# Kernel optimization log

Hardware: AMD Instinct MI355X
Metric: run time of the kernel (lower is better)

The kernel has to match this reference:

```python
import jax, jax.numpy as jnp
import numpy as np

TOP_K = 32
TEMPERATURE = 1.0
PARAM_SCALE = 0.02


def setup_inputs() -> dict:
    key = jax.random.key(0)
    ks = jax.random.split(key, 7)
    B, S, D, F, P, R = 2, 1024, 1024, 4096, 256, 64
    x = jax.random.normal(ks[0], (B, S, D), dtype=jnp.float32)
    fc1_A = jax.random.normal(ks[1], (P, D, R), dtype=jnp.float32) * PARAM_SCALE
    fc1_B = jax.random.normal(ks[2], (P, R, F), dtype=jnp.float32) * PARAM_SCALE
    fc2_A = jax.random.normal(ks[3], (P, F, R), dtype=jnp.float32) * PARAM_SCALE
    fc2_B = jax.random.normal(ks[4], (P, R, D), dtype=jnp.float32) * PARAM_SCALE
    fc1_logits = jax.random.normal(ks[5], (P,), dtype=jnp.float32)
    fc2_logits = jax.random.normal(ks[6], (P,), dtype=jnp.float32)
    return {"x": x, "fc1_A": fc1_A, "fc1_B": fc1_B, "fc2_A": fc2_A,
            "fc2_B": fc2_B, "fc1_logits": fc1_logits, "fc2_logits": fc2_logits}


def _compose_weight(logits, A, B):
    """Top-k select primitives, softmax composition weights, weighted low-rank sum.

    A: (P, d_in, r), B: (P, r, d_out) -> W: (d_in, d_out)
    """
    vals, idx = jax.lax.top_k(logits, TOP_K)          # (K,), (K,)
    w = jax.nn.softmax(vals / TEMPERATURE)            # composition weights over selected
    A_sel = A[idx]                                    # (K, d_in, r) gather
    B_sel = B[idx]                                    # (K, r, d_out) gather
    return jnp.einsum('k,kir,kro->io', w, A_sel, B_sel)


def reference(x, fc1_A, fc1_B, fc2_A, fc2_B, fc1_logits, fc2_logits):
    W1 = _compose_weight(fc1_logits, fc1_A, fc1_B)    # (D, F)
    W2 = _compose_weight(fc2_logits, fc2_A, fc2_B)    # (F, D)
    h = jax.nn.gelu(jnp.einsum('bsd,df->bsf', x, W1))
    return jnp.einsum('bsf,fd->bsd', h, W2)
```

## Files before the change

kernel.cpp:

```cpp
#include <hip/hip_runtime.h>
#include <cstdint>
#include <cstddef>

typedef __attribute__((ext_vector_type(8))) short bhalf8;
typedef __attribute__((ext_vector_type(4))) float f32x4;

__device__ __forceinline__ unsigned short f2bf(float f){
    unsigned int u = __float_as_uint(f);
    u += 0x7fffu + ((u >> 16) & 1u);
    return (unsigned short)(u >> 16);
}

__device__ __forceinline__ float gelu_tanh(float x){
    const float c1 = 2.302584f;
    float y  = x + 0.044715f * x * x * x;
    float e  = __builtin_amdgcn_exp2f(c1 * y);
    float r  = __builtin_amdgcn_rcpf(e + 1.0f);
    return x - x * r;
}

__device__ __forceinline__ void async_lds16(const unsigned short* g, unsigned short* l){
    __builtin_amdgcn_global_load_lds(
        (const __attribute__((address_space(1))) void*)g,
        (__attribute__((address_space(3))) void*)l, 16, 0, 0);
}

__global__ void topk_softmax_kernel(const float* __restrict__ lg1,
                                    const float* __restrict__ lg2,
                                    int* __restrict__ idx_out,
                                    float* __restrict__ w_out)
{
    const float* lg = (blockIdx.x == 0) ? lg1 : lg2;
    int*   idxo = idx_out + blockIdx.x * 32;
    float* wo   = w_out   + blockIdx.x * 32;
    const int lane = threadIdx.x;
    float v[4];
    #pragma unroll
    for (int j = 0; j < 4; ++j) v[j] = lg[lane * 4 + j];
    __shared__ float svals[32];
    for (int k = 0; k < 32; ++k){
        float bv = -1e30f; int bi = 0;
        #pragma unroll
        for (int j = 0; j < 4; ++j){
            if (v[j] > bv){ bv = v[j]; bi = lane * 4 + j; }
        }
        for (int off = 32; off > 0; off >>= 1){
            float ov = __shfl_down(bv, off);
            int   oi = __shfl_down(bi, off);
            if (ov > bv){ bv = ov; bi = oi; }
        }
        bi = __shfl(bi, 0);
        if (lane == 0){ svals[k] = bv; idxo[k] = bi; }
        if ((bi >> 2) == lane) v[bi & 3] = -1e30f;
    }
    float sv = svals[lane & 31];
    float e  = expf(sv - svals[0]);
    float s  = e;
    #pragma unroll
    for (int off = 16; off > 0; off >>= 1) s += __shfl_xor(s, off);
    if (lane < 32) wo[lane] = e / s;
}

__global__ void prep_gather_kernel(const float* __restrict__ x,  unsigned short* __restrict__ x16,
                                   const float* __restrict__ fc1A, unsigned short* __restrict__ Ag1,
                                   const float* __restrict__ fc1B, unsigned short* __restrict__ Bt1,
                                   const float* __restrict__ fc2A, unsigned short* __restrict__ Ag2,
                                   const float* __restrict__ fc2B, unsigned short* __restrict__ Bg2t,
                                   const int* __restrict__ idxb, const float* __restrict__ wb)
{
    __shared__ float tile[64][65];
    const int t = threadIdx.x;
    int b = blockIdx.x;

    if (b < 2048){
        int v = b * 256 + t;
        float4 xx = ((const float4*)x)[v];
        ushort4 o; o.x=f2bf(xx.x); o.y=f2bf(xx.y); o.z=f2bf(xx.z); o.w=f2bf(xx.w);
        ((ushort4*)x16)[v] = o;
        return;
    }
    b -= 2048;
    if (b < 10240){
        const float* src; unsigned short* dst; const int* idx; const float* w;
        int Drows, use_scale, v;
        if (b < 2048){ src=fc1A; dst=Ag1; idx=idxb;    w=wb;    Drows=1024; use_scale=1; v=b*256+t; }
        else         { src=fc2A; dst=Ag2; idx=idxb+32; w=wb+32; Drows=4096; use_scale=0; v=(b-2048)*256+t; }
        int c4 = v & 511;
        int d  = v >> 9;
        int k  = c4 >> 4;
        int r4 = c4 & 15;
        int p  = idx[k];
        float sc = use_scale ? w[k] : 1.0f;
        float4 xx = *((const float4*)(src + ((size_t)p * Drows + d) * 64) + r4);
        ushort4 o;
        o.x = f2bf(sc * xx.x); o.y = f2bf(sc * xx.y);
        o.z = f2bf(sc * xx.z); o.w = f2bf(sc * xx.w);
        *(ushort4*)(dst + (size_t)d * 2048 + k * 64 + r4 * 4) = o;
        return;
    }
    b -= 10240;
    const float* src; unsigned short* dst; const int* idx; const float* w;
    int Fcols, use_scale;
    if (b < 2048){ src=fc1B; dst=Bt1;  idx=idxb;    w=wb;    Fcols=4096; use_scale=0; }
    else         { src=fc2B; dst=Bg2t; idx=idxb+32; w=wb+32; Fcols=1024; use_scale=1; b -= 2048; }
    const int k  = b & 31;
    const int f0 = (b >> 5) * 64;
    const int p  = idx[k];
    const float sc = use_scale ? w[k] : 1.0f;
    const int cf = t & 15;
    const int r0 = t >> 4;
    #pragma unroll
    for (int pass = 0; pass < 4; ++pass){
        int r = r0 + pass * 16;
        float4 xx = *((const float4*)(src + ((size_t)p * 64 + r) * Fcols + f0) + cf);
        tile[r][cf * 4 + 0] = xx.x; tile[r][cf * 4 + 1] = xx.y;
        tile[r][cf * 4 + 2] = xx.z; tile[r][cf * 4 + 3] = xx.w;
    }
    __syncthreads();
    const int r4  = t & 15;
    const int fl0 = t >> 4;
    #pragma unroll
    for (int pass = 0; pass < 4; ++pass){
        int fl = fl0 + pass * 16;
        ushort4 o;
        o.x = f2bf(sc * tile[r4 * 4 + 0][fl]);
        o.y = f2bf(sc * tile[r4 * 4 + 1][fl]);
        o.z = f2bf(sc * tile[r4 * 4 + 2][fl]);
        o.w = f2bf(sc * tile[r4 * 4 + 3][fl]);
        *(ushort4*)(dst + (size_t)(f0 + fl) * 2048 + k * 64 + r4 * 4) = o;
    }
}

template<int EPI>
__device__ __forceinline__ void gemm_body(unsigned short* smem,
                                          const unsigned short* __restrict__ A,
                                          const unsigned short* __restrict__ Bt,
                                          void* __restrict__ Cout,
                                          int N, int K, int Kslice, int kbeg,
                                          int bm, int bn)
{
    const int t    = threadIdx.x;
    const int wave = t >> 6;
    const int lane = t & 63;
    const int wr   = (wave >> 1) * 64;
    const int wc   = (wave & 1) * 64;
    const int m16  = lane & 15;
    const int quad = lane >> 4;
    const int srow = t >> 2;
    const int scol = t & 3;

    f32x4 acc[4][4];
    const f32x4 z = {0.f, 0.f, 0.f, 0.f};
    #pragma unroll
    for (int i = 0; i < 4; ++i)
        #pragma unroll
        for (int j = 0; j < 4; ++j) acc[i][j] = z;

    const unsigned short* Arow = A  + (size_t)(bm + srow) * K + scol * 8 + kbeg;
    const unsigned short* Brow = Bt + (size_t)(bn + srow) * K + scol * 8 + kbeg;
    const size_t rstep = (size_t)64 * K;

    auto stage = [&](int slot, int k0){
        unsigned short* s = smem + slot * 16384 + t * 8;
        async_lds16(Arow + k0,              s);
        async_lds16(Arow + rstep + k0,      s + 2048);
        async_lds16(Arow + k0 + 32,         s + 4096);
        async_lds16(Arow + rstep + k0 + 32, s + 6144);
        async_lds16(Brow + k0,              s + 8192);
        async_lds16(Brow + rstep + k0,      s + 10240);
        async_lds16(Brow + k0 + 32,         s + 12288);
        async_lds16(Brow + rstep + k0 + 32, s + 14336);
    };

    const int nIter = Kslice >> 6;

    stage(0, 0);
    asm volatile("s_waitcnt vmcnt(0)" ::: "memory");
    __builtin_amdgcn_s_barrier();

    for (int it = 0; it < nIter; ++it){
        unsigned short* sb = smem + (it & 1) * 16384;
        if (it + 1 < nIter) stage((it + 1) & 1, (it + 1) * 64);

        bhalf8 af0[4], bf0[4], af1[4], bf1[4];
        #pragma unroll
        for (int i = 0; i < 4; ++i){
            af0[i] = *(const bhalf8*)(sb +         (wr + i * 16 + m16) * 32 + quad * 8);
            af1[i] = *(const bhalf8*)(sb + 4096  + (wr + i * 16 + m16) * 32 + quad * 8);
        }
        #pragma unroll
        for (int j = 0; j < 4; ++j){
            bf0[j] = *(const bhalf8*)(sb + 8192  + (wc + j * 16 + m16) * 32 + quad * 8);
            bf1[j] = *(const bhalf8*)(sb + 12288 + (wc + j * 16 + m16) * 32 + quad * 8);
        }

        #pragma unroll
        for (int i = 0; i < 4; ++i)
            #pragma unroll
            for (int j = 0; j < 4; ++j)
                acc[i][j] = __builtin_amdgcn_mfma_f32_16x16x32_bf16(af0[i], bf0[j], acc[i][j], 0, 0, 0);
        #pragma unroll
        for (int i = 0; i < 4; ++i)
            #pragma unroll
            for (int j = 0; j < 4; ++j)
                acc[i][j] = __builtin_amdgcn_mfma_f32_16x16x32_bf16(af1[i], bf1[j], acc[i][j], 0, 0, 0);

        if (it + 1 < nIter){
            asm volatile("s_waitcnt vmcnt(0) lgkmcnt(0)" ::: "memory");
            __builtin_amdgcn_s_barrier();
        }
    }

    #pragma unroll
    for (int i = 0; i < 4; ++i){
        #pragma unroll
        for (int j = 0; j < 4; ++j){
            #pragma unroll
            for (int r = 0; r < 4; ++r){
                int row = bm + wr + i * 16 + quad * 4 + r;
                int col = bn + wc + j * 16 + m16;
                float vv = acc[i][j][r];
                if (EPI == 1) vv = gelu_tanh(vv);
                if (EPI == 2) ((float*)Cout)[(size_t)row * N + col] = vv;
                else ((unsigned short*)Cout)[(size_t)row * N + col] = f2bf(vv);
            }
        }
    }
}

__device__ __forceinline__ int xcd_swz512(int id){ return (id & 7) * 64 + (id >> 3); }

__launch_bounds__(256, 2)
__global__ void gemm13_kernel(const unsigned short* __restrict__ A1,
                              const unsigned short* __restrict__ B1,
                              unsigned short* __restrict__ C1,
                              const unsigned short* __restrict__ A2,
                              const unsigned short* __restrict__ B2,
                              unsigned short* __restrict__ C2)
{
    __shared__ unsigned short smem[2 * 16384];
    int id = xcd_swz512(blockIdx.x);
    if (id < 256){
        gemm_body<0>(smem, A1, B1, C1, 1024, 2048, 2048, 0,
                     (id >> 3) * 128, (id & 7) * 128);
    } else {
        id -= 256;
        gemm_body<0>(smem, A2, B2, C2, 4096, 2048, 2048, 0,
                     (id >> 5) * 128, (id & 31) * 128);
    }
}

__launch_bounds__(256, 2)
__global__ void gemm2_kernel(const unsigned short* __restrict__ A,
                             const unsigned short* __restrict__ Bt,
                             unsigned short* __restrict__ C)
{
    __shared__ unsigned short smem[2 * 16384];
    int id = xcd_swz512(blockIdx.x);
    gemm_body<1>(smem, A, Bt, C, 4096, 1024, 1024, 0,
                 (id >> 5) * 128, (id & 31) * 128);
}

__launch_bounds__(256, 2)
__global__ void gemm4_kernel(const unsigned short* __restrict__ A,
                             const unsigned short* __restrict__ Bt,
                             float* __restrict__ part)
{
    __shared__ unsigned short smem[2 * 16384];
    int id = xcd_swz512(blockIdx.x);
    int bz = id >> 7;
    int r  = id & 127;
    float* Cs = part + (size_t)bz * (2048 * 1024);
    gemm_body<2>(smem, A, Bt, Cs, 1024, 4096, 1024, bz * 1024,
                 (r >> 3) * 128, (r & 7) * 128);
}

__global__ void reduce4_kernel(const float4* __restrict__ p, float4* __restrict__ out)
{
    const int S = 524288;
    int v = blockIdx.x * 256 + threadIdx.x;
    float4 a = p[v], b = p[v + S], c = p[v + 2 * S], d = p[v + 3 * S];
    float4 r;
    r.x = (a.x + b.x) + (c.x + d.x);
    r.y = (a.y + b.y) + (c.y + d.y);
    r.z = (a.z + b.z) + (c.z + d.z);
    r.w = (a.w + b.w) + (c.w + d.w);
    out[v] = r;
}

extern "C" void kernel_launch(void* const* d_in, const int* in_sizes, int n_in,
                              void* d_out, int out_size, void* d_ws, size_t ws_size,
                              hipStream_t stream)
{
    const float* x    = (const float*)d_in[0];
    const float* fc1A = (const float*)d_in[1];
    const float* fc1B = (const float*)d_in[2];
    const float* fc2A = (const float*)d_in[3];
    const float* fc2B = (const float*)d_in[4];
    const float* lg1  = (const float*)d_in[5];
    const float* lg2  = (const float*)d_in[6];
    float* out = (float*)d_out;

    char* ws = (char*)d_ws;
    int*            idxb = (int*)(ws + 0);
    float*          wb   = (float*)(ws + 256);
    char* base = ws + 4096;
    unsigned short* x16  = (unsigned short*)(base);
    unsigned short* Ag1  = (unsigned short*)(base + (4ull  << 20));
    unsigned short* Bt1  = (unsigned short*)(base + (8ull  << 20));
    unsigned short* Ag2  = (unsigned short*)(base + (24ull << 20));
    unsigned short* Bg2t = (unsigned short*)(base + (40ull << 20));
    unsigned short* W1t  = (unsigned short*)(base + (44ull << 20));
    unsigned short* W2t  = (unsigned short*)(base + (52ull << 20));
    unsigned short* hbuf = (unsigned short*)(base + (60ull << 20));
    float*          part = (float*)(base + (76ull << 20));

    topk_softmax_kernel<<<dim3(2), dim3(64), 0, stream>>>(lg1, lg2, idxb, wb);

    prep_gather_kernel<<<dim3(14848), dim3(256), 0, stream>>>(
        x, x16, fc1A, Ag1, fc1B, Bt1, fc2A, Ag2, fc2B, Bg2t, idxb, wb);

    gemm13_kernel<<<dim3(512), dim3(256), 0, stream>>>(Bt1, Ag1, W1t, Bg2t, Ag2, W2t);

    gemm2_kernel<<<dim3(512), dim3(256), 0, stream>>>(x16, W1t, hbuf);

    gemm4_kernel<<<dim3(512), dim3(256), 0, stream>>>(hbuf, W2t, part);

    reduce4_kernel<<<dim3(2048), dim3(256), 0, stream>>>((const float4*)part, (float4*)out);
}
```

Measured before the change: 578.8 us.

## Fuse split-K reduction into last GEMM via atomic tile counters; merge x cast into topk

The x fp32-to-bf16 conversion moves into the top-k kernel's launch, so the gather kernel no longer carries those blocks. The separate reduce kernel is removed: each split-K block of the final GEMM increments a per-tile atomic counter, and the last of the four sums the partials and writes the output. This saves one launch and overlaps the reduction with the GEMM tail. In exchange it adds fences, an atomic per tile and a serialized reduction in the last-arriving block, and it relies on counters reset in the gather kernel.

```diff
diff --git a/kernel.cpp b/kernel.cpp
--- a/kernel.cpp
+++ b/kernel.cpp
@@ -25,19 +25,30 @@
         (__attribute__((address_space(3))) void*)l, 16, 0, 0);
 }
 
-__global__ void topk_softmax_kernel(const float* __restrict__ lg1,
-                                    const float* __restrict__ lg2,
-                                    int* __restrict__ idx_out,
-                                    float* __restrict__ w_out)
-{
-    const float* lg = (blockIdx.x == 0) ? lg1 : lg2;
-    int*   idxo = idx_out + blockIdx.x * 32;
-    float* wo   = w_out   + blockIdx.x * 32;
+__global__ void topk_conv_kernel(const float* __restrict__ lg1,
+                                 const float* __restrict__ lg2,
+                                 int* __restrict__ idx_out,
+                                 float* __restrict__ w_out,
+                                 const float* __restrict__ x,
+                                 unsigned short* __restrict__ x16)
+{
+    __shared__ float svals[32];
+    const int b = blockIdx.x;
+    if (b >= 2){
+        int v = (b - 2) * 256 + threadIdx.x;
+        float4 xx = ((const float4*)x)[v];
+        ushort4 o; o.x=f2bf(xx.x); o.y=f2bf(xx.y); o.z=f2bf(xx.z); o.w=f2bf(xx.w);
+        ((ushort4*)x16)[v] = o;
+        return;
+    }
+    if (threadIdx.x >= 64) return;
+    const float* lg = (b == 0) ? lg1 : lg2;
+    int*   idxo = idx_out + b * 32;
+    float* wo   = w_out   + b * 32;
     const int lane = threadIdx.x;
     float v[4];
     #pragma unroll
     for (int j = 0; j < 4; ++j) v[j] = lg[lane * 4 + j];
-    __shared__ float svals[32];
     for (int k = 0; k < 32; ++k){
         float bv = -1e30f; int bi = 0;
         #pragma unroll
@@ -61,25 +72,19 @@
     if (lane < 32) wo[lane] = e / s;
 }
 
-__global__ void prep_gather_kernel(const float* __restrict__ x,  unsigned short* __restrict__ x16,
-                                   const float* __restrict__ fc1A, unsigned short* __restrict__ Ag1,
-                                   const float* __restrict__ fc1B, unsigned short* __restrict__ Bt1,
-                                   const float* __restrict__ fc2A, unsigned short* __restrict__ Ag2,
-                                   const float* __restrict__ fc2B, unsigned short* __restrict__ Bg2t,
-                                   const int* __restrict__ idxb, const float* __restrict__ wb)
+__global__ void gather_kernel(const float* __restrict__ fc1A, unsigned short* __restrict__ Ag1,
+                              const float* __restrict__ fc1B, unsigned short* __restrict__ Bt1,
+                              const float* __restrict__ fc2A, unsigned short* __restrict__ Ag2,
+                              const float* __restrict__ fc2B, unsigned short* __restrict__ Bg2t,
+                              const int* __restrict__ idxb, const float* __restrict__ wb,
+                              int* __restrict__ cnt)
 {
     __shared__ float tile[64][65];
     const int t = threadIdx.x;
     int b = blockIdx.x;
 
-    if (b < 2048){
-        int v = b * 256 + t;
-        float4 xx = ((const float4*)x)[v];
-        ushort4 o; o.x=f2bf(xx.x); o.y=f2bf(xx.y); o.z=f2bf(xx.z); o.w=f2bf(xx.w);
-        ((ushort4*)x16)[v] = o;
-        return;
-    }
-    b -= 2048;
+    if (b == 0 && t < 128) cnt[t] = 0;
+
     if (b < 10240){
         const float* src; unsigned short* dst; const int* idx; const float* w;
         int Drows, use_scale, v;
@@ -137,7 +142,11 @@
                                           const unsigned short* __restrict__ Bt,
                                           void* __restrict__ Cout,
                                           int N, int K, int Kslice, int kbeg,
-                                          int bm, int bn)
+                                          int bm, int bn,
+                                          float* part = nullptr,
+                                          float* outp = nullptr,
+                                          int* cnt = nullptr,
+                                          int tileid = 0)
 {
     const int t    = threadIdx.x;
     const int wave = t >> 6;
@@ -221,8 +230,36 @@
                 int col = bn + wc + j * 16 + m16;
                 float vv = acc[i][j][r];
                 if (EPI == 1) vv = gelu_tanh(vv);
-                if (EPI == 2) ((float*)Cout)[(size_t)row * N + col] = vv;
+                if (EPI == 4) ((float*)Cout)[(size_t)row * N + col] = vv;
                 else ((unsigned short*)Cout)[(size_t)row * N + col] = f2bf(vv);
+            }
+        }
+    }
+
+    if (EPI == 4){
+        __threadfence();
+        __syncthreads();
+        int* flag = (int*)smem;
+        if (t == 0)
+            *flag = __hip_atomic_fetch_add(&cnt[tileid], 1,
+                                           __ATOMIC_ACQ_REL, __HIP_MEMORY_SCOPE_AGENT);
+        __syncthreads();
+        if (*flag == 3){
+            __threadfence();
+            const float4* p4 = (const float4*)part;
+            float4* o4 = (float4*)outp;
+            const int S4 = 524288;
+            #pragma unroll
+            for (int i2 = 0; i2 < 16; ++i2){
+                int pos = i2 * 256 + t;
+                int g4  = (bm + (pos >> 5)) * 256 + (bn >> 2) + (pos & 31);
+                float4 a = p4[g4], b2 = p4[g4 + S4], c2 = p4[g4 + 2*S4], d2 = p4[g4 + 3*S4];
+                float4 rr;
+                rr.x = (a.x + b2.x) + (c2.x + d2.x);
+                rr.y = (a.y + b2.y) + (c2.y + d2.y);
+                rr.z = (a.z + b2.z) + (c2.z + d2.z);
+                rr.w = (a.w + b2.w) + (c2.w + d2.w);
+                o4[g4] = rr;
             }
         }
     }
@@ -264,28 +301,17 @@
 __launch_bounds__(256, 2)
 __global__ void gemm4_kernel(const unsigned short* __restrict__ A,
                              const unsigned short* __restrict__ Bt,
-                             float* __restrict__ part)
+                             float* __restrict__ part,
+                             float* __restrict__ outp,
+                             int* __restrict__ cnt)
 {
     __shared__ unsigned short smem[2 * 16384];
     int id = xcd_swz512(blockIdx.x);
     int bz = id >> 7;
     int r  = id & 127;
     float* Cs = part + (size_t)bz * (2048 * 1024);
-    gemm_body<2>(smem, A, Bt, Cs, 1024, 4096, 1024, bz * 1024,
-                 (r >> 3) * 128, (r & 7) * 128);
-}
-
-__global__ void reduce4_kernel(const float4* __restrict__ p, float4* __restrict__ out)
-{
-    const int S = 524288;
-    int v = blockIdx.x * 256 + threadIdx.x;
-    float4 a = p[v], b = p[v + S], c = p[v + 2 * S], d = p[v + 3 * S];
-    float4 r;
-    r.x = (a.x + b.x) + (c.x + d.x);
-    r.y = (a.y + b.y) + (c.y + d.y);
-    r.z = (a.z + b.z) + (c.z + d.z);
-    r.w = (a.w + b.w) + (c.w + d.w);
-    out[v] = r;
+    gemm_body<4>(smem, A, Bt, Cs, 1024, 4096, 1024, bz * 1024,
+                 (r >> 3) * 128, (r & 7) * 128, part, outp, cnt, r);
 }
 
 extern "C" void kernel_launch(void* const* d_in, const int* in_sizes, int n_in,
@@ -304,6 +330,7 @@
     char* ws = (char*)d_ws;
     int*            idxb = (int*)(ws + 0);
     float*          wb   = (float*)(ws + 256);
+    int*            cnt  = (int*)(ws + 512);
     char* base = ws + 4096;
     unsigned short* x16  = (unsigned short*)(base);
     unsigned short* Ag1  = (unsigned short*)(base + (4ull  << 20));
@@ -315,16 +342,14 @@
     unsigned short* hbuf = (unsigned short*)(base + (60ull << 20));
     float*          part = (float*)(base + (76ull << 20));
 
-    topk_softmax_kernel<<<dim3(2), dim3(64), 0, stream>>>(lg1, lg2, idxb, wb);
-
-    prep_gather_kernel<<<dim3(14848), dim3(256), 0, stream>>>(
-        x, x16, fc1A, Ag1, fc1B, Bt1, fc2A, Ag2, fc2B, Bg2t, idxb, wb);
+    topk_conv_kernel<<<dim3(2050), dim3(256), 0, stream>>>(lg1, lg2, idxb, wb, x, x16);
+
+    gather_kernel<<<dim3(12800), dim3(256), 0, stream>>>(
+        fc1A, Ag1, fc1B, Bt1, fc2A, Ag2, fc2B, Bg2t, idxb, wb, cnt);
 
     gemm13_kernel<<<dim3(512), dim3(256), 0, stream>>>(Bt1, Ag1, W1t, Bg2t, Ag2, W2t);
 
     gemm2_kernel<<<dim3(512), dim3(256), 0, stream>>>(x16, W1t, hbuf);
 
-    gemm4_kernel<<<dim3(512), dim3(256), 0, stream>>>(hbuf, W2t, part);
-
-    reduce4_kernel<<<dim3(2048), dim3(256), 0, stream>>>((const float4*)part, (float4*)out);
-}
+    gemm4_kernel<<<dim3(512), dim3(256), 0, stream>>>(hbuf, W2t, part, out, cnt);
+}
```

Measured after the change: 684.3 us. 18.2% more time.
